# Kernel optimization log

Measured on AMD Instinct MI355X. Metric: run time of the kernel, lower is better.

## Reference

```python
import jax, jax.numpy as jnp
import numpy as np
import math

B, I, C = 64, 512, 32
PRED, PL, ST, NH = 96, 16, 8, 8
WKS = (24, 168, 336)
PN = (I + ST - PL) // ST + 1  # 64 patches (padding_patch='end')

def _gelu(x):
    return jax.nn.gelu(x, approximate=False)  # torch nn.GELU default (erf)

def _ln(x, g, b, eps=1e-5):
    m = x.mean(-1, keepdims=True)
    v = ((x - m) ** 2).mean(-1, keepdims=True)
    return (x - m) / jnp.sqrt(v + eps) * g + b

def setup_inputs() -> dict:
    keys = jax.random.split(jax.random.key(0), 64)
    ki = iter(keys)
    def nrm(sh, sc=0.02):
        return (jax.random.normal(next(ki), sh) * sc).astype(jnp.float32)
    inp = {}
    inp['s'] = jax.random.normal(next(ki), (B, I, C), jnp.float32)
    inp['t'] = jax.random.normal(next(ki), (B, I, C), jnp.float32)
    inp['cycle_index'] = jax.random.randint(next(ki), (B,), 0, 336)
    # router: Linear(C, C//2) -> GELU -> Linear(C//2, num_scales)
    inp['rw1'] = nrm((C // 2, C)); inp['rb1'] = jnp.zeros(C // 2)
    inp['rw2'] = nrm((3, C // 2)); inp['rb2'] = jnp.zeros(3)
    # per-scale amplitude / phase tables (Wk, C)
    inp['A0'] = nrm((WKS[0], C), 1.0); inp['A1'] = nrm((WKS[1], C), 1.0); inp['A2'] = nrm((WKS[2], C), 1.0)
    inp['P0'] = (jax.random.uniform(next(ki), (WKS[0], C)) * 2 * math.pi).astype(jnp.float32)
    inp['P1'] = (jax.random.uniform(next(ki), (WKS[1], C)) * 2 * math.pi).astype(jnp.float32)
    inp['P2'] = (jax.random.uniform(next(ki), (WKS[2], C)) * 2 * math.pi).astype(jnp.float32)
    # PB_RPA (phase-biased relative patch attention), n_embd=PL, n_head=NH
    inp['Wqkv'] = nrm((3 * PL, PL)); inp['bqkv'] = jnp.zeros(3 * PL)
    inp['Wo'] = nrm((PL, PL)); inp['bo'] = jnp.zeros(PL)
    inp['alpha'] = jnp.ones(())
    # bn2 over channel dim = patch_num
    inp['bn_g'] = jnp.ones(PN); inp['bn_b'] = jnp.zeros(PN)
    inp['W3'] = nrm((2 * PRED, PN * PL)); inp['b3'] = jnp.zeros(2 * PRED)
    inp['W4'] = nrm((PRED, 2 * PRED)); inp['b4'] = jnp.zeros(PRED)
    inp['W5'] = nrm((4 * PRED, I)); inp['b5'] = jnp.zeros(4 * PRED)
    inp['W6'] = nrm((PRED, 2 * PRED)); inp['b6'] = jnp.zeros(PRED)
    inp['W7'] = nrm((PRED, PRED // 2)); inp['b7'] = jnp.zeros(PRED)
    inp['W8'] = nrm((PRED, 2 * PRED)); inp['b8'] = jnp.zeros(PRED)
    inp['ln1_g'] = jnp.ones(2 * PRED); inp['ln1_b'] = jnp.zeros(2 * PRED)
    inp['ln2_g'] = jnp.ones(PRED // 2); inp['ln2_b'] = jnp.zeros(PRED // 2)
    # TrendEnhancer: Conv1d(C, C, 3, pad=1) gated residual
    inp['te_w'] = nrm((C, C, 3)); inp['te_b'] = jnp.zeros(C)
    return inp

def _forward(s, t, cycle_index, rw1, rb1, rw2, rb2, A0, A1, A2, P0, P1, P2,
             Wqkv, bqkv, Wo, bo, alpha, bn_g, bn_b, W3, b3, W4, b4, W5, b5,
             W6, b6, W7, b7, W8, b8, ln1_g, ln1_b, ln2_g, ln2_b, te_w, te_b):
    s = s.transpose(0, 2, 1)  # (B,C,I)
    t = t.transpose(0, 2, 1)
    # router -> per-scale softmax weights (B, num_scales)
    h = _gelu(s.mean(-1) @ rw1.T + rb1)
    p = jax.nn.softmax(h @ rw2.T + rb2, axis=-1)
    ar = jnp.arange(I)
    cs, ps = [], []
    for Atab, Ptab, Wk in ((A0, P0, WKS[0]), (A1, P1, WKS[1]), (A2, P2, WKS[2])):
        idx = (cycle_index[:, None] + ar) % Wk            # (B,I) data-dependent gather
        A = jax.nn.softplus(Atab[idx]).transpose(0, 2, 1)  # (B,C,I)
        phi = Ptab[idx].transpose(0, 2, 1)
        Qr = A * jnp.cos(phi)                              # Qi=A*sin(phi) is unused in hermitian_attn
        S = jnp.einsum('bcl,bck->blk', Qr, s) / math.sqrt(C)
        Aw = jax.nn.softmax(S, axis=-1)
        cs.append(jnp.einsum('blk,bck->bcl', Aw, s))
        ps.append(phi)
    c_stack = jnp.stack(cs, 1)    # (B,3,C,I)
    phi_stack = jnp.stack(ps, 1)
    beta = p[:, :, None, None]
    s = s + (beta * c_stack).sum(1)
    fused_phi = (beta * phi_stack).sum(1)  # (B,C,I)
    N = B * C
    s = s.reshape(N, I)
    t = t.reshape(N, I)
    phi = jnp.repeat(fused_phi.mean(1), C, axis=0)  # (N,I)
    # padding_patch='end' -> replicate-pad last `stride` steps
    s = jnp.concatenate([s, jnp.repeat(s[:, -1:], ST, 1)], 1)
    phi = jnp.concatenate([phi, jnp.repeat(phi[:, -1:], ST, 1)], 1)
    widx = jnp.arange(PN)[:, None] * ST + jnp.arange(PL)
    sp = s[:, widx]                # (N, PN, PL) unfold
    phis = phi[:, widx].mean(-1)   # (N, PN)
    # PB_RPA: MHA over patches with phase-difference bias
    qkv = sp @ Wqkv.T + bqkv
    q, k, v = jnp.split(qkv, 3, axis=-1)
    hd = PL // NH
    def heads(x):
        return x.reshape(N, PN, NH, hd).transpose(0, 2, 1, 3)
    q, k, v = heads(q), heads(k), heads(v)
    bias = alpha * jnp.cos(phis[:, None, :, None] - phis[:, None, None, :])  # (N,1,PN,PN)
    sc = jnp.einsum('nhtd,nhsd->nhts', q, k) / math.sqrt(hd) + bias
    Aw = jax.nn.softmax(sc, axis=-1)
    o = jnp.einsum('nhts,nhsd->nhtd', Aw, v).transpose(0, 2, 1, 3).reshape(N, PN, PL)
    o = o @ Wo.T + bo
    sx = _gelu(sp + o)
    # bn2: BatchNorm1d over channel=patch_num (training-mode batch stats)
    mu = sx.mean((0, 2), keepdims=True)
    var = ((sx - mu) ** 2).mean((0, 2), keepdims=True)
    sx = (sx - mu) / jnp.sqrt(var + 1e-5) * bn_g[None, :, None] + bn_b[None, :, None]
    sx = sx.reshape(N, PN * PL)
    sx = _gelu(sx @ W3.T + b3) @ W4.T + b4  # (N, PRED)
    # trend branch
    u = t @ W5.T + b5                       # (N, 4*PRED)
    u = u.reshape(N, 2 * PRED, 2).mean(-1)  # AvgPool1d(2)
    u = _ln(u, ln1_g, ln1_b)
    u = u @ W6.T + b6
    u = u.reshape(N, PRED // 2, 2).mean(-1)
    u = _ln(u, ln2_g, ln2_b)
    u = u @ W7.T + b7                       # (N, PRED)
    u = u.reshape(B, C, PRED)
    f = jnp.fft.rfft(u, axis=-1)
    mask = (jnp.arange(f.shape[-1]) < 5).astype(f.dtype)
    u = u + jnp.fft.irfft(f * mask, n=PRED, axis=-1)
    y = jax.lax.conv_general_dilated(u, te_w, (1,), [(1, 1)],
                                     dimension_numbers=('NCH', 'OIH', 'NCH')) + te_b[None, :, None]
    u = (u + _gelu(y)).reshape(N, PRED)     # TrendEnhancer gated-conv residual
    x = jnp.concatenate([sx, u], 1) @ W8.T + b8
    return x.reshape(B, C, PRED).transpose(0, 2, 1)  # (B, pred_len, C)

def reference(s, t, cycle_index, rw1, rb1, rw2, rb2, A0, A1, A2, P0, P1, P2,
              Wqkv, bqkv, Wo, bo, alpha, bn_g, bn_b, W3, b3, W4, b4, W5, b5,
              W6, b6, W7, b7, W8, b8, ln1_g, ln1_b, ln2_g, ln2_b, te_w, te_b):
    return _forward(s, t, cycle_index, rw1, rb1, rw2, rb2, A0, A1, A2, P0, P1, P2,
                    Wqkv, bqkv, Wo, bo, alpha, bn_g, bn_b, W3, b3, W4, b4, W5, b5,
                    W6, b6, W7, b7, W8, b8, ln1_g, ln1_b, ln2_g, ln2_b, te_w, te_b)
```

## Files before the change

### kernel.cpp

```cpp
#include <hip/hip_runtime.h>
#include <math.h>

#define B_    64
#define I_    512
#define C_    32
#define PRED_ 96
#define PL_   16
#define ST_   8
#define NH_   8
#define PN_   64
#define N_    2048

typedef short bf16x8 __attribute__((ext_vector_type(8)));
typedef float f32x4 __attribute__((ext_vector_type(4)));
typedef bf16x8 __attribute__((may_alias)) bf16x8_a;
typedef uint2 __attribute__((may_alias)) uint2_a;
typedef uint4 __attribute__((may_alias)) uint4_a;

__device__ __forceinline__ float geluf(float x) {
    return 0.5f * x * (1.0f + erff(x * 0.70710678118654752f));
}
__device__ __forceinline__ float softplusf(float x) {
    return fmaxf(x, 0.0f) + log1pf(__expf(-fabsf(x)));
}
__device__ __forceinline__ unsigned short f2bf(float x) {
    union { float f; unsigned int u; } v; v.f = x;
    unsigned int r = v.u + 0x7fffu + ((v.u >> 16) & 1u);
    return (unsigned short)(r >> 16);
}

__global__ void k_headphi(const float* __restrict__ s, const float* __restrict__ rw1,
                          const float* __restrict__ rb1, const float* __restrict__ rw2,
                          const float* __restrict__ rb2,
                          const float* __restrict__ P0, const float* __restrict__ P1,
                          const float* __restrict__ P2, const int* __restrict__ cyc,
                          float* __restrict__ wp, float* __restrict__ phis) {
    int b = blockIdx.x, t = threadIdx.x;
    __shared__ float part[8][32];
    __shared__ float smean[32];
    __shared__ float h[16];
    __shared__ float wpl[3];
    __shared__ float pm[I_];
    int c = t & 31, chunk = t >> 5;
    float acc = 0.f;
    for (int l = chunk * 64; l < chunk * 64 + 64; ++l)
        acc += s[((size_t)b * I_ + l) * C_ + c];
    part[chunk][c] = acc;
    __syncthreads();
    if (t < 32) {
        float v = 0.f;
#pragma unroll
        for (int i = 0; i < 8; ++i) v += part[i][t];
        smean[t] = v * (1.0f / I_);
    }
    __syncthreads();
    if (t < 16) {
        float a = rb1[t];
#pragma unroll
        for (int c2 = 0; c2 < 32; ++c2) a += smean[c2] * rw1[t * 32 + c2];
        h[t] = geluf(a);
    }
    __syncthreads();
    if (t == 0) {
        float lg[3], mx = -1e30f;
        for (int k = 0; k < 3; ++k) {
            float a = rb2[k];
            for (int j = 0; j < 16; ++j) a += h[j] * rw2[k * 16 + j];
            lg[k] = a; mx = fmaxf(mx, a);
        }
        float d = 0.f;
        for (int k = 0; k < 3; ++k) { lg[k] = __expf(lg[k] - mx); d += lg[k]; }
        float inv = 1.f / d;
        for (int k = 0; k < 3; ++k) { wpl[k] = lg[k] * inv; wp[b * 3 + k] = lg[k] * inv; }
    }
    __syncthreads();
    float p0 = wpl[0], p1 = wpl[1], p2 = wpl[2];
    int cy = cyc[b];
    for (int l = t; l < I_; l += 256) {
        float acc2 = 0.f;
        {
            int idx = (cy + l) % 24;
            const float4* r = (const float4*)(P0 + idx * 32);
            float s4 = 0.f;
#pragma unroll
            for (int i = 0; i < 8; ++i) { float4 v = r[i]; s4 += v.x + v.y + v.z + v.w; }
            acc2 += p0 * s4;
        }
        {
            int idx = (cy + l) % 168;
            const float4* r = (const float4*)(P1 + idx * 32);
            float s4 = 0.f;
#pragma unroll
            for (int i = 0; i < 8; ++i) { float4 v = r[i]; s4 += v.x + v.y + v.z + v.w; }
            acc2 += p1 * s4;
        }
        {
            int idx = (cy + l) % 336;
            const float4* r = (const float4*)(P2 + idx * 32);
            float s4 = 0.f;
#pragma unroll
            for (int i = 0; i < 8; ++i) { float4 v = r[i]; s4 += v.x + v.y + v.z + v.w; }
            acc2 += p2 * s4;
        }
        pm[l] = acc2 * (1.0f / 32.0f);
    }
    __syncthreads();
    if (t < PN_) {
        float sum = 0.f;
#pragma unroll
        for (int j = 0; j < 16; ++j) {
            int l = t * ST_ + j; if (l > 511) l = 511;
            sum += pm[l];
        }
        phis[b * PN_ + t] = sum * (1.0f / 16.0f);
    }
}

__global__ void __launch_bounds__(512) k_attn_mfma(
        const float* __restrict__ s, const int* __restrict__ cyc,
        const float* __restrict__ A0, const float* __restrict__ A1, const float* __restrict__ A2,
        const float* __restrict__ P0, const float* __restrict__ P1, const float* __restrict__ P2,
        const float* __restrict__ wp, float* __restrict__ pcs) {
    int k3 = blockIdx.x, b = blockIdx.y;
    int t = threadIdx.x;
    int wid = t >> 6, lane = t & 63;
    int l15 = lane & 15, lg = lane >> 4;

    __shared__ unsigned short s_lds[512][40];
    __shared__ unsigned short sT[32][520];
    __shared__ unsigned short Pt[8][64][40];

    {
        int row = t;
        const float4* src = (const float4*)(s + ((size_t)b * I_ + row) * C_);
        unsigned short bv[32];
#pragma unroll
        for (int i = 0; i < 8; ++i) {
            float4 v = src[i];
            bv[4 * i + 0] = f2bf(v.x); bv[4 * i + 1] = f2bf(v.y);
            bv[4 * i + 2] = f2bf(v.z); bv[4 * i + 3] = f2bf(v.w);
        }
#pragma unroll
        for (int i = 0; i < 4; ++i) {
            uint4 pk;
            pk.x = (unsigned)bv[8 * i + 0] | ((unsigned)bv[8 * i + 1] << 16);
            pk.y = (unsigned)bv[8 * i + 2] | ((unsigned)bv[8 * i + 3] << 16);
            pk.z = (unsigned)bv[8 * i + 4] | ((unsigned)bv[8 * i + 5] << 16);
            pk.w = (unsigned)bv[8 * i + 6] | ((unsigned)bv[8 * i + 7] << 16);
            *((uint4_a*)&s_lds[row][8 * i]) = pk;
        }
#pragma unroll
        for (int cc = 0; cc < 32; ++cc) sT[cc][row] = bv[cc];
    }

    const float* Atab; const float* Ptab; int Wk;
    if (k3 == 0)      { Atab = A0; Ptab = P0; Wk = 24;  }
    else if (k3 == 1) { Atab = A1; Ptab = P1; Wk = 168; }
    else              { Atab = A2; Ptab = P2; Wk = 336; }
    float wpv = wp[b * 3 + k3];
    int cy = cyc[b];
    bf16x8 qrf[4];
#pragma unroll
    for (int qt = 0; qt < 4; ++qt) {
        int q = wid * 64 + qt * 16 + l15;
        int idx = (cy + q) % Wk;
        const float4* Ar = (const float4*)(Atab + idx * 32 + lg * 8);
        const float4* Pr = (const float4*)(Ptab + idx * 32 + lg * 8);
        float4 a0 = Ar[0], a1 = Ar[1], p0 = Pr[0], p1 = Pr[1];
        float qv[8];
        qv[0] = softplusf(a0.x) * __cosf(p0.x);
        qv[1] = softplusf(a0.y) * __cosf(p0.y);
        qv[2] = softplusf(a0.z) * __cosf(p0.z);
        qv[3] = softplusf(a0.w) * __cosf(p0.w);
        qv[4] = softplusf(a1.x) * __cosf(p1.x);
        qv[5] = softplusf(a1.y) * __cosf(p1.y);
        qv[6] = softplusf(a1.z) * __cosf(p1.z);
        qv[7] = softplusf(a1.w) * __cosf(p1.w);
        bf16x8 f;
#pragma unroll
        for (int j = 0; j < 8; ++j) f[j] = (short)f2bf(qv[j]);
        qrf[qt] = f;
    }
    __syncthreads();

    const float rs = 0.17677669529663687f;
    f32x4 acc[4][2];
#pragma unroll
    for (int qt = 0; qt < 4; ++qt)
#pragma unroll
        for (int ct = 0; ct < 2; ++ct) acc[qt][ct] = (f32x4){0.f, 0.f, 0.f, 0.f};
    float dacc[4] = {0.f, 0.f, 0.f, 0.f};

    for (int kc = 0; kc < 16; ++kc) {
        int key0 = kc * 32;
        bf16x8 a0 = *((const bf16x8_a*)&s_lds[key0 + l15][lg * 8]);
        bf16x8 a1 = *((const bf16x8_a*)&s_lds[key0 + 16 + l15][lg * 8]);
        f32x4 stv[4][2];
#pragma unroll
        for (int qt = 0; qt < 4; ++qt) {
            stv[qt][0] = __builtin_amdgcn_mfma_f32_16x16x32_bf16(a0, qrf[qt], (f32x4){0.f,0.f,0.f,0.f}, 0, 0, 0);
            stv[qt][1] = __builtin_amdgcn_mfma_f32_16x16x32_bf16(a1, qrf[qt], (f32x4){0.f,0.f,0.f,0.f}, 0, 0, 0);
        }
#pragma unroll
        for (int qt = 0; qt < 4; ++qt) {
#pragma unroll
            for (int h = 0; h < 2; ++h) {
                unsigned short pb[4];
                float ds = 0.f;
#pragma unroll
                for (int r = 0; r < 4; ++r) {
                    float e = __expf(stv[qt][h][r] * rs);
                    unsigned short ub = f2bf(e);
                    pb[r] = ub;
                    union { unsigned int u; float f; } bb; bb.u = ((unsigned int)ub) << 16;
                    ds += bb.f;
                }
                dacc[qt] += ds;
                uint2 w2;
                w2.x = (unsigned)pb[0] | ((unsigned)pb[1] << 16);
                w2.y = (unsigned)pb[2] | ((unsigned)pb[3] << 16);
                *((uint2_a*)&Pt[wid][qt * 16 + l15][h * 16 + lg * 4]) = w2;
            }
        }
        bf16x8 b0 = *((const bf16x8_a*)&sT[l15][key0 + lg * 8]);
        bf16x8 b1 = *((const bf16x8_a*)&sT[16 + l15][key0 + lg * 8]);
#pragma unroll
        for (int qt = 0; qt < 4; ++qt) {
            bf16x8 pa = *((const bf16x8_a*)&Pt[wid][qt * 16 + l15][lg * 8]);
            acc[qt][0] = __builtin_amdgcn_mfma_f32_16x16x32_bf16(pa, b0, acc[qt][0], 0, 0, 0);
            acc[qt][1] = __builtin_amdgcn_mfma_f32_16x16x32_bf16(pa, b1, acc[qt][1], 0, 0, 0);
        }
    }

#pragma unroll
    for (int qt = 0; qt < 4; ++qt) {
        float dq = dacc[qt];
        dq += __shfl_xor(dq, 16);
        dq += __shfl_xor(dq, 32);
        float invd[4];
#pragma unroll
        for (int r = 0; r < 4; ++r) {
            float dr = __shfl(dq, 4 * lg + r);
            invd[r] = wpv / dr;
        }
        int qbase = wid * 64 + qt * 16 + 4 * lg;
#pragma unroll
        for (int ct = 0; ct < 2; ++ct) {
            int c = ct * 16 + l15;
            float4 o;
            o.x = acc[qt][ct][0] * invd[0];
            o.y = acc[qt][ct][1] * invd[1];
            o.z = acc[qt][ct][2] * invd[2];
            o.w = acc[qt][ct][3] * invd[3];
            *(float4*)(pcs + (((size_t)k3 * B_ + b) * C_ + c) * I_ + qbase) = o;
        }
    }
}

__global__ void k_combine(const float* __restrict__ s, const float* __restrict__ pcs,
                          float* __restrict__ srow) {
    int b = blockIdx.x, l0 = blockIdx.y * 32;
    int tt_ = threadIdx.x;
    __shared__ float st[32][33];
#pragma unroll
    for (int r = 0; r < 4; ++r) {
        int lin = r * 256 + tt_;
        int lq = lin >> 5, c = lin & 31;
        st[lq][c] = s[((size_t)b * I_ + l0 + lq) * C_ + c];
    }
    __syncthreads();
    const size_t CH = (size_t)B_ * C_ * I_;
#pragma unroll
    for (int r = 0; r < 4; ++r) {
        int lin = r * 256 + tt_;
        int co = lin >> 5, lo = lin & 31;
        size_t pi = ((size_t)b * C_ + co) * I_ + l0 + lo;
        float sum = pcs[pi] + pcs[CH + pi] + pcs[2 * CH + pi];
        srow[pi] = st[lo][co] + sum;
    }
}

__global__ void __launch_bounds__(256) k_patch(
        const float* __restrict__ srow, const float* __restrict__ phis,
        const float* __restrict__ Wqkv, const float* __restrict__ bqkv,
        const float* __restrict__ Wo, const float* __restrict__ bo,
        const float* __restrict__ alpha_p, float* __restrict__ sx) {
    int n = blockIdx.x, t = threadIdx.x;
    int p = t & 63, w = t >> 6;
    int lane = t & 63, l15 = lane & 15, lg = lane >> 4;
    int b = n >> 5;
    __shared__ float spl[64][17];
    __shared__ unsigned short spb[64][16];
    __shared__ unsigned short wqb[48][16];
    __shared__ unsigned short qkv2[36][72];
    __shared__ float vlf[16][68];
    __shared__ float o2l[64][18];
    __shared__ float wo[16][16];
    const float rs2 = 0.70710678118654752f;

    float alpha = alpha_p[0];
    const float* srn = srow + (size_t)n * I_;
#pragma unroll
    for (int jj = 0; jj < 4; ++jj) {
        int j = w * 4 + jj;
        int l = p * ST_ + j; if (l > 511) l = 511;
        float v = srn[l];
        spl[p][j] = v; spb[p][j] = f2bf(v);
    }
    for (int i = t; i < 768; i += 256) wqb[i >> 4][i & 15] = f2bf(Wqkv[i]);
    wo[t >> 4][t & 15] = Wo[t];
    if (t < 64) {
        float sv, cv;
        __sincosf(phis[b * PN_ + t], &sv, &cv);
        qkv2[32][t] = f2bf(cv); qkv2[33][t] = f2bf(sv);
        qkv2[34][t] = f2bf(alpha * cv); qkv2[35][t] = f2bf(alpha * sv);
    }
    __syncthreads();

    {
        bf16x8 af = {};
        if (lg < 2) af = *((const bf16x8_a*)&spb[w * 16 + l15][lg * 8]);
        f32x4 pacc[3];
#pragma unroll
        for (int nt = 0; nt < 3; ++nt) {
            bf16x8 wf = {};
            if (lg < 2) wf = *((const bf16x8_a*)&wqb[nt * 16 + l15][lg * 8]);
            pacc[nt] = __builtin_amdgcn_mfma_f32_16x16x32_bf16(af, wf, (f32x4){0.f,0.f,0.f,0.f}, 0, 0, 0);
        }
        __syncthreads();
#pragma unroll
        for (int nt = 0; nt < 3; ++nt) {
            int o = nt * 16 + l15;
            float bias = bqkv[o];
            float v0 = pacc[nt][0] + bias, v1 = pacc[nt][1] + bias;
            float v2 = pacc[nt][2] + bias, v3 = pacc[nt][3] + bias;
            int pb_ = w * 16 + 4 * lg;
            if (o < 16) {
                v0 *= rs2; v1 *= rs2; v2 *= rs2; v3 *= rs2;
                uint2 w2;
                w2.x = (unsigned)f2bf(v0) | ((unsigned)f2bf(v1) << 16);
                w2.y = (unsigned)f2bf(v2) | ((unsigned)f2bf(v3) << 16);
                *((uint2_a*)&qkv2[o][pb_]) = w2;
            } else if (o < 32) {
                uint2 w2;
                w2.x = (unsigned)f2bf(v0) | ((unsigned)f2bf(v1) << 16);
                w2.y = (unsigned)f2bf(v2) | ((unsigned)f2bf(v3) << 16);
                *((uint2_a*)&qkv2[o][pb_]) = w2;
            } else {
                *(float4*)&vlf[o - 32][pb_] = make_float4(v0, v1, v2, v3);
            }
        }
    }
    __syncthreads();

#pragma unroll
    for (int hh = 0; hh < 2; ++hh) {
        int h = 2 * w + hh;
        bf16x8 qf[4];
#pragma unroll
        for (int pt = 0; pt < 4; ++pt) {
            bf16x8 f = {};
            if (lg == 0) {
                int col = pt * 16 + l15;
                f[0] = (short)qkv2[2 * h][col];
                f[1] = (short)qkv2[2 * h + 1][col];
                f[2] = (short)qkv2[34][col];
                f[3] = (short)qkv2[35][col];
            }
            qf[pt] = f;
        }
        float o0a[4] = {0.f,0.f,0.f,0.f}, o1a[4] = {0.f,0.f,0.f,0.f}, da[4] = {0.f,0.f,0.f,0.f};
#pragma unroll
        for (int st = 0; st < 4; ++st) {
            bf16x8 kf = {};
            if (lg == 0) {
                int col = st * 16 + l15;
                kf[0] = (short)qkv2[16 + 2 * h][col];
                kf[1] = (short)qkv2[17 + 2 * h][col];
                kf[2] = (short)qkv2[32][col];
                kf[3] = (short)qkv2[33][col];
            }
            float4 v0 = *(const float4*)&vlf[2 * h][st * 16 + 4 * lg];
            float4 v1 = *(const float4*)&vlf[2 * h + 1][st * 16 + 4 * lg];
#pragma unroll
            for (int pt = 0; pt < 4; ++pt) {
                f32x4 sv = __builtin_amdgcn_mfma_f32_16x16x32_bf16(kf, qf[pt], (f32x4){0.f,0.f,0.f,0.f}, 0, 0, 0);
                float e0 = __expf(sv[0]), e1 = __expf(sv[1]);
                float e2 = __expf(sv[2]), e3 = __expf(sv[3]);
                da[pt] += e0 + e1 + e2 + e3;
                o0a[pt] += e0 * v0.x + e1 * v0.y + e2 * v0.z + e3 * v0.w;
                o1a[pt] += e0 * v1.x + e1 * v1.y + e2 * v1.z + e3 * v1.w;
            }
        }
#pragma unroll
        for (int pt = 0; pt < 4; ++pt) {
            float o0 = o0a[pt], o1 = o1a[pt], dd = da[pt];
            o0 += __shfl_xor(o0, 16); o0 += __shfl_xor(o0, 32);
            o1 += __shfl_xor(o1, 16); o1 += __shfl_xor(o1, 32);
            dd += __shfl_xor(dd, 16); dd += __shfl_xor(dd, 32);
            if (lg == 0) {
                float inv = 1.f / dd;
                *(float2*)&o2l[pt * 16 + l15][2 * h] = make_float2(o0 * inv, o1 * inv);
            }
        }
    }
    __syncthreads();

    float* sxr = sx + ((size_t)n * PN_ + p) * PL_;
#pragma unroll
    for (int ii = 0; ii < 4; ++ii) {
        int i2 = w * 4 + ii;
        float a = bo[i2];
#pragma unroll
        for (int j = 0; j < 16; ++j) a += o2l[p][j] * wo[i2][j];
        sxr[i2] = geluf(spl[p][i2] + a);
    }
}

__global__ void k_bn_stats(const float* __restrict__ sx, float* __restrict__ bnpart) {
    int pn = blockIdx.x, chunk = blockIdx.y, t = threadIdx.x;
    __shared__ float r1[256], r2[256];
    int j4 = t & 3, nb = t >> 2;
    float s1 = 0.f, s2 = 0.f;
    for (int i = 0; i < 8; ++i) {
        int n = chunk * 512 + nb + i * 64;
        float4 v = *(const float4*)(sx + ((size_t)n * PN_ + pn) * PL_ + j4 * 4);
        s1 += v.x + v.y + v.z + v.w;
        s2 += v.x * v.x + v.y * v.y + v.z * v.z + v.w * v.w;
    }
    r1[t] = s1; r2[t] = s2;
    __syncthreads();
    for (int st = 128; st > 0; st >>= 1) {
        if (t < st) { r1[t] += r1[t + st]; r2[t] += r2[t + st]; }
        __syncthreads();
    }
    if (t == 0) {
        bnpart[(pn * 4 + chunk) * 2 + 0] = r1[0];
        bnpart[(pn * 4 + chunk) * 2 + 1] = r2[0];
    }
}

template <int ACT, int FUSE_BN, int TRANS>
__global__ void __launch_bounds__(256) k_gemm_mfma(
        const float* __restrict__ A, const float* __restrict__ W,
        const float* __restrict__ bias, const float* __restrict__ bnpart,
        const float* __restrict__ bng, const float* __restrict__ bnb,
        float* __restrict__ Cout, int M, int Nn, int K) {
    __shared__ unsigned short Ab[64][36];
    __shared__ unsigned short Wb[64][36];
    __shared__ float bnm[64], bna[64];
    int bm = blockIdx.x * 64, bn = blockIdx.y * 64;
    int t = threadIdx.x;
    int wid = t >> 6, lane = t & 63, l15 = lane & 15, lg = lane >> 4;
    int srw = t >> 2, sk = (t & 3) * 8;
    if (FUSE_BN && t < 64) {
        float s1 = 0.f, s2 = 0.f;
#pragma unroll
        for (int ch = 0; ch < 4; ++ch) {
            s1 += bnpart[(t * 4 + ch) * 2 + 0];
            s2 += bnpart[(t * 4 + ch) * 2 + 1];
        }
        const float inv = 1.0f / (N_ * PL_);
        float mu = s1 * inv;
        float var = s2 * inv - mu * mu;
        float m = rsqrtf(var + 1e-5f) * bng[t];
        bnm[t] = m; bna[t] = bnb[t] - mu * m;
    }
    if (FUSE_BN) __syncthreads();
    f32x4 acc[4];
#pragma unroll
    for (int nt = 0; nt < 4; ++nt) acc[nt] = (f32x4){0.f, 0.f, 0.f, 0.f};

    for (int kt = 0; kt < K; kt += 32) {
        float4 av0, av1;
        if (TRANS) {
            int nrow = bm + srw;
            const float* tp = A + (size_t)(nrow >> 5) * (I_ * C_) + (nrow & 31);
            int l0 = kt + sk;
            av0.x = tp[(size_t)(l0 + 0) * C_]; av0.y = tp[(size_t)(l0 + 1) * C_];
            av0.z = tp[(size_t)(l0 + 2) * C_]; av0.w = tp[(size_t)(l0 + 3) * C_];
            av1.x = tp[(size_t)(l0 + 4) * C_]; av1.y = tp[(size_t)(l0 + 5) * C_];
            av1.z = tp[(size_t)(l0 + 6) * C_]; av1.w = tp[(size_t)(l0 + 7) * C_];
        } else {
            av0 = *(const float4*)(A + (size_t)(bm + srw) * K + kt + sk);
            av1 = *(const float4*)(A + (size_t)(bm + srw) * K + kt + sk + 4);
        }
        float4 wv0 = *(const float4*)(W + (size_t)(bn + srw) * K + kt + sk);
        float4 wv1 = *(const float4*)(W + (size_t)(bn + srw) * K + kt + sk + 4);
        if (FUSE_BN) {
            int pn = (kt + sk) >> 4;
            float m = bnm[pn], ad = bna[pn];
            av0.x = av0.x * m + ad; av0.y = av0.y * m + ad;
            av0.z = av0.z * m + ad; av0.w = av0.w * m + ad;
            av1.x = av1.x * m + ad; av1.y = av1.y * m + ad;
            av1.z = av1.z * m + ad; av1.w = av1.w * m + ad;
        }
        __syncthreads();
        {
            uint4 pk;
            pk.x = (unsigned)f2bf(av0.x) | ((unsigned)f2bf(av0.y) << 16);
            pk.y = (unsigned)f2bf(av0.z) | ((unsigned)f2bf(av0.w) << 16);
            pk.z = (unsigned)f2bf(av1.x) | ((unsigned)f2bf(av1.y) << 16);
            pk.w = (unsigned)f2bf(av1.z) | ((unsigned)f2bf(av1.w) << 16);
            *((uint4_a*)&Ab[srw][sk]) = pk;
            uint4 pw;
            pw.x = (unsigned)f2bf(wv0.x) | ((unsigned)f2bf(wv0.y) << 16);
            pw.y = (unsigned)f2bf(wv0.z) | ((unsigned)f2bf(wv0.w) << 16);
            pw.z = (unsigned)f2bf(wv1.x) | ((unsigned)f2bf(wv1.y) << 16);
            pw.w = (unsigned)f2bf(wv1.z) | ((unsigned)f2bf(wv1.w) << 16);
            *((uint4_a*)&Wb[srw][sk]) = pw;
        }
        __syncthreads();
        bf16x8 af = *((const bf16x8_a*)&Ab[wid * 16 + l15][lg * 8]);
#pragma unroll
        for (int nt = 0; nt < 4; ++nt) {
            bf16x8 wf = *((const bf16x8_a*)&Wb[nt * 16 + l15][lg * 8]);
            acc[nt] = __builtin_amdgcn_mfma_f32_16x16x32_bf16(af, wf, acc[nt], 0, 0, 0);
        }
    }
#pragma unroll
    for (int nt = 0; nt < 4; ++nt) {
#pragma unroll
        for (int r = 0; r < 4; ++r) {
            int m_ = bm + wid * 16 + 4 * lg + r;
            int n_ = bn + nt * 16 + l15;
            float v = acc[nt][r] + bias[n_];
            if (ACT) v = geluf(v);
            Cout[(size_t)m_ * Nn + n_] = v;
        }
    }
}

__global__ void k_rowmlp4(const float* __restrict__ g3, const float* __restrict__ W4,
                          const float* __restrict__ b4, float* __restrict__ sxf) {
    int n = blockIdx.x, t = threadIdx.x;
    __shared__ float row[192];
    for (int j = t; j < 192; j += 128) row[j] = g3[(size_t)n * 192 + j];
    __syncthreads();
    if (t < 96) {
        float a = b4[t];
        const float* wr = W4 + t * 192;
#pragma unroll 4
        for (int j = 0; j < 192; ++j) a += row[j] * wr[j];
        sxf[(size_t)n * 96 + t] = a;
    }
}

__global__ void k_u(const float* __restrict__ u1, const float* __restrict__ ln1g,
                    const float* __restrict__ ln1b, const float* __restrict__ W6,
                    const float* __restrict__ b6, const float* __restrict__ ln2g,
                    const float* __restrict__ ln2b, const float* __restrict__ W7,
                    const float* __restrict__ b7, float* __restrict__ u2out) {
    int n = blockIdx.x, t = threadIdx.x;
    __shared__ float a[192];
    __shared__ float red1[256], red2[256];
    __shared__ float c2[48];
    __shared__ float stat[2];
    __shared__ float u3l[96];
    __shared__ float cosb[5][96], sinb[5][96];
    __shared__ float coef[9];
    if (t < 96) {
#pragma unroll
        for (int k = 0; k < 5; ++k) {
            float sv, cv2;
            __sincosf(6.283185307179586f * (float)(k * t) / 96.0f, &sv, &cv2);
            cosb[k][t] = cv2; sinb[k][t] = sv;
        }
    }
    const float* ur = u1 + (size_t)n * 384;
    float av = 0.5f * (ur[2 * t] + ur[2 * t + 1]);
    red1[t] = av; red2[t] = av * av;
    if (t < 64) { red1[192 + t] = 0.f; red2[192 + t] = 0.f; }
    __syncthreads();
    for (int st = 128; st > 0; st >>= 1) {
        if (t < st) { red1[t] += red1[t + st]; red2[t] += red2[t + st]; }
        __syncthreads();
    }
    if (t == 0) {
        float mu = red1[0] * (1.0f / 192.0f);
        float var = red2[0] * (1.0f / 192.0f) - mu * mu;
        stat[0] = mu; stat[1] = rsqrtf(var + 1e-5f);
    }
    __syncthreads();
    a[t] = (av - stat[0]) * stat[1] * ln1g[t] + ln1b[t];
    __syncthreads();
    float bv = 0.f;
    if (t < 96) {
        bv = b6[t];
        const float* wr = W6 + t * 192;
#pragma unroll 4
        for (int j = 0; j < 192; ++j) bv += a[j] * wr[j];
    }
    __syncthreads();
    if (t < 96) red1[t] = bv;
    __syncthreads();
    float cv = 0.f;
    if (t < 48) cv = 0.5f * (red1[2 * t] + red1[2 * t + 1]);
    __syncthreads();
    if (t < 48) { red1[t] = cv; red2[t] = cv * cv; }
    else if (t < 64) { red1[t] = 0.f; red2[t] = 0.f; }
    __syncthreads();
    for (int st = 32; st > 0; st >>= 1) {
        if (t < st) { red1[t] += red1[t + st]; red2[t] += red2[t + st]; }
        __syncthreads();
    }
    if (t == 0) {
        float mu = red1[0] * (1.0f / 48.0f);
        float var = red2[0] * (1.0f / 48.0f) - mu * mu;
        stat[0] = mu; stat[1] = rsqrtf(var + 1e-5f);
    }
    __syncthreads();
    if (t < 48) c2[t] = (cv - stat[0]) * stat[1] * ln2g[t] + ln2b[t];
    __syncthreads();
    if (t < 96) {
        float acc = b7[t];
        const float* wr = W7 + t * 48;
#pragma unroll
        for (int j = 0; j < 48; ++j) acc += c2[j] * wr[j];
        u3l[t] = acc;
    }
    __syncthreads();
    if (t < 9) {
        int k = (t < 5) ? t : t - 4;
        const float* bas = (t < 5) ? cosb[k] : sinb[k];
        float acc = 0.f;
#pragma unroll 4
        for (int m = 0; m < 96; ++m) acc += u3l[m] * bas[m];
        coef[t] = acc;
    }
    __syncthreads();
    if (t < 96) {
        float rec = coef[0];
#pragma unroll
        for (int k = 1; k <= 4; ++k)
            rec += 2.0f * (coef[k] * cosb[k][t] + coef[4 + k] * sinb[k][t]);
        u2out[(size_t)n * 96 + t] = u3l[t] + rec * (1.0f / 96.0f);
    }
}

__global__ void k_conv(const float* __restrict__ u2, const float* __restrict__ tw,
                       const float* __restrict__ tb, float* __restrict__ u4) {
    int b = blockIdx.x, xq = blockIdx.y, t = threadIdx.x;
    int x0 = xq * 24;
    __shared__ float ub[32][26];
    __shared__ float twl[3072];
    for (int i = t; i < 832; i += 256) {
        int ic = i / 26, xx = i % 26;
        int gx = x0 + xx - 1;
        ub[ic][xx] = (gx >= 0 && gx < 96) ? u2[((size_t)b * 32 + ic) * 96 + gx] : 0.f;
    }
    for (int i = t; i < 3072; i += 256) twl[i] = tw[i];
    __syncthreads();
    for (int i = t; i < 768; i += 256) {
        int oc = i / 24, xx = i % 24;
        float acc = tb[oc];
#pragma unroll 8
        for (int ic = 0; ic < 32; ++ic) {
            const float* wv = twl + (oc * 32 + ic) * 3;
            acc += ub[ic][xx] * wv[0] + ub[ic][xx + 1] * wv[1] + ub[ic][xx + 2] * wv[2];
        }
        u4[((size_t)b * 32 + oc) * 96 + x0 + xx] = ub[oc][xx + 1] + geluf(acc);
    }
}

__global__ void k_out(const float* __restrict__ sxf, const float* __restrict__ u4,
                      const float* __restrict__ W8, const float* __restrict__ b8,
                      float* __restrict__ out) {
    int b = blockIdx.x, oq = blockIdx.y, t = threadIdx.x;
    __shared__ float ld[32][193];
    for (int i = t; i < 32 * 96; i += 256) {
        int c = i / 96, j = i % 96;
        ld[c][j]      = sxf[((size_t)(b * 32 + c)) * 96 + j];
        ld[c][96 + j] = u4[((size_t)(b * 32 + c)) * 96 + j];
    }
    __syncthreads();
    for (int i = t; i < 24 * 32; i += 256) {
        int o = oq * 24 + (i >> 5), c = i & 31;
        float acc = b8[o];
        const float* wr = W8 + o * 192;
#pragma unroll 4
        for (int j = 0; j < 192; ++j) acc += ld[c][j] * wr[j];
        out[((size_t)b * 96 + o) * 32 + c] = acc;
    }
}

extern "C" void kernel_launch(void* const* d_in, const int* in_sizes, int n_in,
                              void* d_out, int out_size, void* d_ws, size_t ws_size,
                              hipStream_t stream) {
    const float* s    = (const float*)d_in[0];
    const float* t    = (const float*)d_in[1];
    const int*   cyc  = (const int*)d_in[2];
    const float* rw1  = (const float*)d_in[3];
    const float* rb1  = (const float*)d_in[4];
    const float* rw2  = (const float*)d_in[5];
    const float* rb2  = (const float*)d_in[6];
    const float* A0   = (const float*)d_in[7];
    const float* A1   = (const float*)d_in[8];
    const float* A2   = (const float*)d_in[9];
    const float* P0   = (const float*)d_in[10];
    const float* P1   = (const float*)d_in[11];
    const float* P2   = (const float*)d_in[12];
    const float* Wqkv = (const float*)d_in[13];
    const float* bqkv = (const float*)d_in[14];
    const float* Wo   = (const float*)d_in[15];
    const float* bo   = (const float*)d_in[16];
    const float* alpha= (const float*)d_in[17];
    const float* bn_g = (const float*)d_in[18];
    const float* bn_b = (const float*)d_in[19];
    const float* W3   = (const float*)d_in[20];
    const float* b3   = (const float*)d_in[21];
    const float* W4   = (const float*)d_in[22];
    const float* b4   = (const float*)d_in[23];
    const float* W5   = (const float*)d_in[24];
    const float* b5   = (const float*)d_in[25];
    const float* W6   = (const float*)d_in[26];
    const float* b6   = (const float*)d_in[27];
    const float* W7   = (const float*)d_in[28];
    const float* b7   = (const float*)d_in[29];
    const float* W8   = (const float*)d_in[30];
    const float* b8   = (const float*)d_in[31];
    const float* ln1g = (const float*)d_in[32];
    const float* ln1b = (const float*)d_in[33];
    const float* ln2g = (const float*)d_in[34];
    const float* ln2b = (const float*)d_in[35];
    const float* tew  = (const float*)d_in[36];
    const float* teb  = (const float*)d_in[37];

    float* ws     = (float*)d_ws;
    float* wp     = ws;
    float* phis   = ws + 192;
    float* bnpart = ws + 4288;
    float* srow   = ws + 4800;
    float* R      = srow + 1048576;
    float* pcs = R;
    float* sx  = R;
    float* g3  = R + 2097152;
    float* sxf = R + 2490368;
    float* u1  = R + 2686976;
    float* u2f = R + 3473408;
    float* u4f = R + 3670016;
    float* out = (float*)d_out;

    k_headphi<<<64, 256, 0, stream>>>(s, rw1, rb1, rw2, rb2, P0, P1, P2, cyc, wp, phis);
    k_attn_mfma<<<dim3(3, 64), 512, 0, stream>>>(s, cyc, A0, A1, A2, P0, P1, P2, wp, pcs);
    k_combine<<<dim3(64, 16), 256, 0, stream>>>(s, pcs, srow);
    k_patch<<<2048, 256, 0, stream>>>(srow, phis, Wqkv, bqkv, Wo, bo, alpha, sx);
    k_bn_stats<<<dim3(64, 4), 256, 0, stream>>>(sx, bnpart);
    k_gemm_mfma<1, 1, 0><<<dim3(32, 3), 256, 0, stream>>>(sx, W3, b3, bnpart, bn_g, bn_b, g3, 2048, 192, 1024);
    k_rowmlp4<<<2048, 128, 0, stream>>>(g3, W4, b4, sxf);
    k_gemm_mfma<0, 0, 1><<<dim3(32, 6), 256, 0, stream>>>(t, W5, b5, bnpart, bn_g, bn_b, u1, 2048, 384, 512);
    k_u<<<2048, 192, 0, stream>>>(u1, ln1g, ln1b, W6, b6, ln2g, ln2b, W7, b7, u2f);
    k_conv<<<dim3(64, 4), 256, 0, stream>>>(u2f, tew, teb, u4f);
    k_out<<<dim3(64, 4), 256, 0, stream>>>(sxf, u4f, W8, b8, out);
}
```

Measured before the change: 341.8 us.

## Split attention key range across two blocks and normalize in combine kernel

The attention kernel now splits the 512 keys into two halves handled by separate blocks, doubling the grid from 192 to 384 blocks. Each block writes unnormalized partial sums and softmax denominators, and k_combine merges the halves, applies the router weight divided by the total denominator, and sums the scales. The loop also interleaves the score MFMA, exp and PV MFMA per query tile, which shrinks the per-wave P scratch and LDS use. In exchange, the intermediate pcs buffer doubles and the combine kernel reads more global memory.

```diff
diff --git a/kernel.cpp b/kernel.cpp
--- a/kernel.cpp
+++ b/kernel.cpp
@@ -120,44 +120,45 @@
         const float* __restrict__ s, const int* __restrict__ cyc,
         const float* __restrict__ A0, const float* __restrict__ A1, const float* __restrict__ A2,
         const float* __restrict__ P0, const float* __restrict__ P1, const float* __restrict__ P2,
-        const float* __restrict__ wp, float* __restrict__ pcs) {
-    int k3 = blockIdx.x, b = blockIdx.y;
+        float* __restrict__ pd, float* __restrict__ pcs) {
+    int bx = blockIdx.x;
+    int k3 = bx >> 1, kh = bx & 1;
+    int b = blockIdx.y;
     int t = threadIdx.x;
     int wid = t >> 6, lane = t & 63;
     int l15 = lane & 15, lg = lane >> 4;
 
-    __shared__ unsigned short s_lds[512][40];
-    __shared__ unsigned short sT[32][520];
-    __shared__ unsigned short Pt[8][64][40];
+    __shared__ unsigned short s_lds[256][36];
+    __shared__ unsigned short sT[32][262];
+    __shared__ unsigned short Pt[8][16][36];
 
     {
-        int row = t;
-        const float4* src = (const float4*)(s + ((size_t)b * I_ + row) * C_);
-        unsigned short bv[32];
-#pragma unroll
-        for (int i = 0; i < 8; ++i) {
+        int row = t >> 1, half = t & 1;
+        const float4* src = (const float4*)(s + ((size_t)b * I_ + kh * 256 + row) * C_ + half * 16);
+        unsigned short bv[16];
+#pragma unroll
+        for (int i = 0; i < 4; ++i) {
             float4 v = src[i];
             bv[4 * i + 0] = f2bf(v.x); bv[4 * i + 1] = f2bf(v.y);
             bv[4 * i + 2] = f2bf(v.z); bv[4 * i + 3] = f2bf(v.w);
         }
 #pragma unroll
-        for (int i = 0; i < 4; ++i) {
+        for (int i = 0; i < 2; ++i) {
             uint4 pk;
             pk.x = (unsigned)bv[8 * i + 0] | ((unsigned)bv[8 * i + 1] << 16);
             pk.y = (unsigned)bv[8 * i + 2] | ((unsigned)bv[8 * i + 3] << 16);
             pk.z = (unsigned)bv[8 * i + 4] | ((unsigned)bv[8 * i + 5] << 16);
             pk.w = (unsigned)bv[8 * i + 6] | ((unsigned)bv[8 * i + 7] << 16);
-            *((uint4_a*)&s_lds[row][8 * i]) = pk;
-        }
-#pragma unroll
-        for (int cc = 0; cc < 32; ++cc) sT[cc][row] = bv[cc];
+            *((uint4_a*)&s_lds[row][half * 16 + 8 * i]) = pk;
+        }
+#pragma unroll
+        for (int cc = 0; cc < 16; ++cc) sT[half * 16 + cc][row] = bv[cc];
     }
 
     const float* Atab; const float* Ptab; int Wk;
     if (k3 == 0)      { Atab = A0; Ptab = P0; Wk = 24;  }
     else if (k3 == 1) { Atab = A1; Ptab = P1; Wk = 168; }
     else              { Atab = A2; Ptab = P2; Wk = 336; }
-    float wpv = wp[b * 3 + k3];
     int cy = cyc[b];
     bf16x8 qrf[4];
 #pragma unroll
@@ -191,25 +192,24 @@
         for (int ct = 0; ct < 2; ++ct) acc[qt][ct] = (f32x4){0.f, 0.f, 0.f, 0.f};
     float dacc[4] = {0.f, 0.f, 0.f, 0.f};
 
-    for (int kc = 0; kc < 16; ++kc) {
+    for (int kc = 0; kc < 8; ++kc) {
         int key0 = kc * 32;
         bf16x8 a0 = *((const bf16x8_a*)&s_lds[key0 + l15][lg * 8]);
         bf16x8 a1 = *((const bf16x8_a*)&s_lds[key0 + 16 + l15][lg * 8]);
-        f32x4 stv[4][2];
+        bf16x8 b0 = *((const bf16x8_a*)&sT[l15][key0 + lg * 8]);
+        bf16x8 b1 = *((const bf16x8_a*)&sT[16 + l15][key0 + lg * 8]);
 #pragma unroll
         for (int qt = 0; qt < 4; ++qt) {
-            stv[qt][0] = __builtin_amdgcn_mfma_f32_16x16x32_bf16(a0, qrf[qt], (f32x4){0.f,0.f,0.f,0.f}, 0, 0, 0);
-            stv[qt][1] = __builtin_amdgcn_mfma_f32_16x16x32_bf16(a1, qrf[qt], (f32x4){0.f,0.f,0.f,0.f}, 0, 0, 0);
-        }
-#pragma unroll
-        for (int qt = 0; qt < 4; ++qt) {
+            f32x4 st0 = __builtin_amdgcn_mfma_f32_16x16x32_bf16(a0, qrf[qt], (f32x4){0.f,0.f,0.f,0.f}, 0, 0, 0);
+            f32x4 st1 = __builtin_amdgcn_mfma_f32_16x16x32_bf16(a1, qrf[qt], (f32x4){0.f,0.f,0.f,0.f}, 0, 0, 0);
 #pragma unroll
             for (int h = 0; h < 2; ++h) {
+                f32x4 sv = h ? st1 : st0;
                 unsigned short pb[4];
                 float ds = 0.f;
 #pragma unroll
                 for (int r = 0; r < 4; ++r) {
-                    float e = __expf(stv[qt][h][r] * rs);
+                    float e = __expf(sv[r] * rs);
                     unsigned short ub = f2bf(e);
                     pb[r] = ub;
                     union { unsigned int u; float f; } bb; bb.u = ((unsigned int)ub) << 16;
@@ -219,55 +219,53 @@
                 uint2 w2;
                 w2.x = (unsigned)pb[0] | ((unsigned)pb[1] << 16);
                 w2.y = (unsigned)pb[2] | ((unsigned)pb[3] << 16);
-                *((uint2_a*)&Pt[wid][qt * 16 + l15][h * 16 + lg * 4]) = w2;
+                *((uint2_a*)&Pt[wid][l15][h * 16 + lg * 4]) = w2;
             }
-        }
-        bf16x8 b0 = *((const bf16x8_a*)&sT[l15][key0 + lg * 8]);
-        bf16x8 b1 = *((const bf16x8_a*)&sT[16 + l15][key0 + lg * 8]);
-#pragma unroll
-        for (int qt = 0; qt < 4; ++qt) {
-            bf16x8 pa = *((const bf16x8_a*)&Pt[wid][qt * 16 + l15][lg * 8]);
+            bf16x8 pa = *((const bf16x8_a*)&Pt[wid][l15][lg * 8]);
             acc[qt][0] = __builtin_amdgcn_mfma_f32_16x16x32_bf16(pa, b0, acc[qt][0], 0, 0, 0);
             acc[qt][1] = __builtin_amdgcn_mfma_f32_16x16x32_bf16(pa, b1, acc[qt][1], 0, 0, 0);
         }
     }
 
+    int hh = k3 * 2 + kh;
 #pragma unroll
     for (int qt = 0; qt < 4; ++qt) {
         float dq = dacc[qt];
         dq += __shfl_xor(dq, 16);
         dq += __shfl_xor(dq, 32);
-        float invd[4];
-#pragma unroll
-        for (int r = 0; r < 4; ++r) {
-            float dr = __shfl(dq, 4 * lg + r);
-            invd[r] = wpv / dr;
-        }
+        int q = wid * 64 + qt * 16 + l15;
+        if (lg == 0) pd[((size_t)hh * B_ + b) * I_ + q] = dq;
         int qbase = wid * 64 + qt * 16 + 4 * lg;
 #pragma unroll
         for (int ct = 0; ct < 2; ++ct) {
             int c = ct * 16 + l15;
             float4 o;
-            o.x = acc[qt][ct][0] * invd[0];
-            o.y = acc[qt][ct][1] * invd[1];
-            o.z = acc[qt][ct][2] * invd[2];
-            o.w = acc[qt][ct][3] * invd[3];
-            *(float4*)(pcs + (((size_t)k3 * B_ + b) * C_ + c) * I_ + qbase) = o;
-        }
-    }
-}
-
-__global__ void k_combine(const float* __restrict__ s, const float* __restrict__ pcs,
+            o.x = acc[qt][ct][0]; o.y = acc[qt][ct][1];
+            o.z = acc[qt][ct][2]; o.w = acc[qt][ct][3];
+            *(float4*)(pcs + (((size_t)hh * B_ + b) * C_ + c) * I_ + qbase) = o;
+        }
+    }
+}
+
+__global__ void k_combine(const float* __restrict__ s, const float* __restrict__ pd,
+                          const float* __restrict__ pcs, const float* __restrict__ wp,
                           float* __restrict__ srow) {
     int b = blockIdx.x, l0 = blockIdx.y * 32;
     int tt_ = threadIdx.x;
     __shared__ float st[32][33];
+    __shared__ float rw[3][32];
 #pragma unroll
     for (int r = 0; r < 4; ++r) {
         int lin = r * 256 + tt_;
         int lq = lin >> 5, c = lin & 31;
         st[lq][c] = s[((size_t)b * I_ + l0 + lq) * C_ + c];
     }
+    if (tt_ < 96) {
+        int k3 = tt_ >> 5, lq = tt_ & 31;
+        float d = pd[((size_t)(k3 * 2 + 0) * B_ + b) * I_ + l0 + lq]
+                + pd[((size_t)(k3 * 2 + 1) * B_ + b) * I_ + l0 + lq];
+        rw[k3][lq] = wp[b * 3 + k3] / d;
+    }
     __syncthreads();
     const size_t CH = (size_t)B_ * C_ * I_;
 #pragma unroll
@@ -275,7 +273,12 @@
         int lin = r * 256 + tt_;
         int co = lin >> 5, lo = lin & 31;
         size_t pi = ((size_t)b * C_ + co) * I_ + l0 + lo;
-        float sum = pcs[pi] + pcs[CH + pi] + pcs[2 * CH + pi];
+        float sum = 0.f;
+#pragma unroll
+        for (int k3 = 0; k3 < 3; ++k3) {
+            float v = pcs[(2 * k3) * CH + pi] + pcs[(2 * k3 + 1) * CH + pi];
+            sum += rw[k3][lo] * v;
+        }
         srow[pi] = st[lo][co] + sum;
     }
 }
@@ -732,7 +735,8 @@
     float* bnpart = ws + 4288;
     float* srow   = ws + 4800;
     float* R      = srow + 1048576;
-    float* pcs = R;
+    float* pd  = R;
+    float* pcs = R + 196608;
     float* sx  = R;
     float* g3  = R + 2097152;
     float* sxf = R + 2490368;
@@ -742,8 +746,8 @@
     float* out = (float*)d_out;
 
     k_headphi<<<64, 256, 0, stream>>>(s, rw1, rb1, rw2, rb2, P0, P1, P2, cyc, wp, phis);
-    k_attn_mfma<<<dim3(3, 64), 512, 0, stream>>>(s, cyc, A0, A1, A2, P0, P1, P2, wp, pcs);
-    k_combine<<<dim3(64, 16), 256, 0, stream>>>(s, pcs, srow);
+    k_attn_mfma<<<dim3(6, 64), 512, 0, stream>>>(s, cyc, A0, A1, A2, P0, P1, P2, pd, pcs);
+    k_combine<<<dim3(64, 16), 256, 0, stream>>>(s, pd, pcs, wp, srow);
     k_patch<<<2048, 256, 0, stream>>>(srow, phis, Wqkv, bqkv, Wo, bo, alpha, sx);
     k_bn_stats<<<dim3(64, 4), 256, 0, stream>>>(sx, bnpart);
     k_gemm_mfma<1, 1, 0><<<dim3(32, 3), 256, 0, stream>>>(sx, W3, b3, bnpart, bn_g, bn_b, g3, 2048, 192, 1024);
```

Result: slower. 355.7 us (+4.0%).
